# Kernel tuning notes

Measured on AMD Instinct MI355X. Metric: run time of the kernel, lower is better.

Reference implementation:

```python
import jax, jax.numpy as jnp
import numpy as np

N = 131072      # total nodes
B = 16          # graphs in batch (num_segments)
C = 128         # in_channels
K = 16          # n_super_nodes
TAU = 1.0
PRUNING_THRESHOLD = 0.01
SPARSITY_WEIGHT = 0.01
TEMPORAL_W = 0.1 * 5
COLLAPSE_W = 2.0
EPS = 1e-9


def setup_inputs() -> dict:
    key = jax.random.key(0)
    ks = jax.random.split(key, 8)
    x = jax.random.normal(ks[0], (N, C), dtype=jnp.float32)
    batch = jnp.sort(jax.random.randint(ks[1], (N,), 0, B)).astype(jnp.int64)
    pos = jax.random.normal(ks[2], (N, 2), dtype=jnp.float32)
    # Gumbel noise for gumbel_softmax (sampled once, passed as input for determinism)
    gumbel = jax.random.gumbel(ks[3], (N, K), dtype=jnp.float32)
    # assign_mlp params: Linear(C,C) -> ReLU -> Linear(C,K)
    W1 = jax.random.normal(ks[4], (C, C), dtype=jnp.float32) / np.sqrt(C)
    b1 = jnp.zeros((C,), dtype=jnp.float32)
    W2 = jax.random.normal(ks[5], (K, C), dtype=jnp.float32) / np.sqrt(C)
    b2 = jnp.zeros((K,), dtype=jnp.float32)
    scaling = jnp.asarray(10.0, dtype=jnp.float32)
    active_mask = jnp.ones((K,), dtype=jnp.float32)  # buffer, starts all-active
    return {"x": x, "batch": batch, "pos": pos, "gumbel": gumbel,
            "W1": W1, "b1": b1, "W2": W2, "b2": b2,
            "scaling": scaling, "active_mask": active_mask}


def reference(x, batch, pos, gumbel, W1, b1, W2, b2, scaling, active_mask):
    # --- assignment logits: MLP * scaling (eval mode, prev_assignments=None) ---
    h = jax.nn.relu(x @ W1.T + b1)            # [N, C]
    logits = (h @ W2.T + b2) * scaling        # [N, K]
    # eval-path masking: masked_fill(mask == 0, -1e9)
    masked_logits = jnp.where(active_mask[None, :] == 0.0, -1e9, logits)
    # gumbel_softmax (soft, hard=False)
    s = jax.nn.softmax((masked_logits + gumbel) / TAU, axis=-1)   # [N, K]

    avg_s = jnp.mean(s, axis=0)               # [K]

    # --- losses ---
    entropy = -jnp.mean(jnp.sum(s * jnp.log(s + EPS), axis=1))
    uniform_p = 1.0 / K
    diversity = jnp.sum(uniform_p * jnp.log(uniform_p / (avg_s + EPS)))
    pruning = jnp.mean(jnp.abs(avg_s * (1.0 - active_mask)))
    sparsity = (jnp.sum(active_mask) / K) * SPARSITY_WEIGHT
    temporal = jnp.asarray(0.0, jnp.float32)  # prev_assignments is None
    # collapse-prevention / balance bodies are truncated upstream; faithful proxies
    collapse = jnp.sum((avg_s - uniform_p) ** 2) * COLLAPSE_W
    balance = jnp.std(avg_s)
    spatial = jnp.asarray(0.0, jnp.float32)

    # --- pooled features: out[b,k,c] = sum_{n in graph b} s[n,k] * x[n,c] ---
    weighted = x[:, None, :] * s[:, :, None]                  # [N, K, C]
    out = jax.ops.segment_sum(weighted, batch, num_segments=B)  # [B, K, C]

    # --- super-node positions ---
    w_pos = pos[:, None, :] * s[:, :, None]                    # [N, K, 2]
    sum_s_pos = jax.ops.segment_sum(w_pos, batch, num_segments=B)  # [B, K, 2]
    sum_s = jax.ops.segment_sum(s, batch, num_segments=B)[..., None] + EPS  # [B, K, 1]
    mu = sum_s_pos / sum_s                                     # [B, K, 2]

    # --- separation loss: pairwise repulsion between super-node centers ---
    dist_sq = jnp.sum((mu[:, :, None, :] - mu[:, None, :, :]) ** 2, axis=-1)  # [B,K,K]
    eye = jnp.eye(K, dtype=mu.dtype)[None]
    repulsion = 1.0 / (dist_sq + 1.0)
    separation = jnp.sum(repulsion * (1.0 - eye)) / (K * (K - 1))

    losses = jnp.stack([entropy, diversity, spatial, pruning, sparsity,
                        temporal * TEMPORAL_W, collapse, balance, separation])
    return out, s, mu, losses
```

## Files before the change

kernel.cpp:

```cpp
#include <hip/hip_runtime.h>
#include <hip/hip_bf16.h>
#include <math.h>

#define NN 131072
#define BSEG 16
#define CCH 128
#define KK 16
#define EPSF 1e-9f
#define XST 136

#define OFF_S   32768
#define OFF_MU  2129920
#define OFF_L   2130432

#define REDC_BASE 1024
#define REDC_STRIDE 1024
#define NRED 64
#define ST_BASE (REDC_BASE + NRED * REDC_STRIDE)
#define NST 4
#define ST_SZ (BSEG * KK * CCH)

typedef __bf16 bf16x8 __attribute__((ext_vector_type(8)));
typedef float  f32x4  __attribute__((ext_vector_type(4)));
typedef float  f32x16 __attribute__((ext_vector_type(16)));

__device__ __forceinline__ int load_batch(const void* bptr, int n, int is64) {
    if (is64) return (int)((const long long*)bptr)[n];
    return ((const int*)bptr)[n];
}

__device__ __forceinline__ float wave_sum(float v) {
#pragma unroll
    for (int o = 32; o > 0; o >>= 1) v += __shfl_xor(v, o, 64);
    return v;
}

__device__ __forceinline__ bf16x8 pack8(float4 a, float4 b) {
    bf16x8 v;
    v[0] = (__bf16)a.x; v[1] = (__bf16)a.y; v[2] = (__bf16)a.z; v[3] = (__bf16)a.w;
    v[4] = (__bf16)b.x; v[5] = (__bf16)b.y; v[6] = (__bf16)b.z; v[7] = (__bf16)b.w;
    return v;
}

__global__ void k_zero(float* __restrict__ ws, const int* __restrict__ b32) {
    int i = blockIdx.x * 256 + threadIdx.x;
    ws[REDC_BASE + i] = 0.0f;
    if (i == 0) ws[0] = (b32[NN - 1] == 0) ? 1.0f : 0.0f;
}

__global__ __launch_bounds__(256, 2) void k_fused(
    const float* __restrict__ x, const void* __restrict__ batch,
    const float* __restrict__ pos, const float* __restrict__ gumbel,
    const float* __restrict__ W1, const float* __restrict__ b1,
    const float* __restrict__ W2, const float* __restrict__ b2,
    const float* __restrict__ scaling, const float* __restrict__ active_mask,
    float* __restrict__ s_out, float* __restrict__ ws)
{
    __shared__ __align__(16) __bf16 x_lds[128 * XST];
    __shared__ __align__(16) __bf16 h_lds[128 * XST];
    __shared__ __align__(16) __bf16 sT[16 * XST];
    __shared__ int bsegs[128];

    const int tid  = threadIdx.x;
    const int lane = tid & 63;
    const int wv   = tid >> 6;
    const int n0   = blockIdx.x * 128;
    const int is64 = (int)ws[0];

    if (tid < 128) bsegs[tid] = load_batch(batch, n0 + tid, is64);

    float4 ga0, ga1, ga2, ga3;
    if (tid < 128) {
        const float4* gp = (const float4*)(gumbel + (size_t)(n0 + tid) * KK);
        ga0 = gp[0]; ga1 = gp[1]; ga2 = gp[2]; ga3 = gp[3];
    }

    {
        const float4* xg = (const float4*)(x + (size_t)n0 * CCH);
#pragma unroll
        for (int i = 0; i < 8; i++) {
            int p = i * 256 + tid;
            float4 a = xg[2 * p], b = xg[2 * p + 1];
            *(bf16x8*)&x_lds[(p >> 4) * XST + (p & 15) * 8] = pack8(a, b);
        }
    }
    __syncthreads();

    {
        bf16x8 bfr[8];
        const float* wrow = W1 + (size_t)(wv * 32 + (lane & 31)) * CCH + (lane >> 5) * 8;
#pragma unroll
        for (int ks = 0; ks < 8; ks++) {
            float4 u = *(const float4*)(wrow + ks * 16);
            float4 v = *(const float4*)(wrow + ks * 16 + 4);
            bfr[ks] = pack8(u, v);
        }
        f32x16 acc[4];
#pragma unroll
        for (int mt = 0; mt < 4; mt++)
#pragma unroll
            for (int r = 0; r < 16; r++) acc[mt][r] = 0.0f;

#pragma unroll
        for (int ks = 0; ks < 8; ks++) {
#pragma unroll
            for (int mt = 0; mt < 4; mt++) {
                bf16x8 a = *(bf16x8*)&x_lds[(size_t)(mt * 32 + (lane & 31)) * XST + ks * 16 + (lane >> 5) * 8];
                acc[mt] = __builtin_amdgcn_mfma_f32_32x32x16_bf16(a, bfr[ks], acc[mt], 0, 0, 0);
            }
        }
        const float b1j = b1[wv * 32 + (lane & 31)];
#pragma unroll
        for (int mt = 0; mt < 4; mt++)
#pragma unroll
            for (int r = 0; r < 16; r++) {
                int node = mt * 32 + (r & 3) + 8 * (r >> 2) + 4 * (lane >> 5);
                h_lds[(size_t)node * XST + wv * 32 + (lane & 31)] = (__bf16)fmaxf(acc[mt][r] + b1j, 0.0f);
            }
    }
    __syncthreads();

    {
        f32x4 acc2[2];
#pragma unroll
        for (int t = 0; t < 2; t++)
#pragma unroll
            for (int r = 0; r < 4; r++) acc2[t][r] = 0.0f;

#pragma unroll
        for (int ks = 0; ks < 4; ks++) {
            const float* w2row = W2 + (size_t)(lane & 15) * CCH + ks * 32 + (lane >> 4) * 8;
            float4 u = *(const float4*)w2row;
            float4 v = *(const float4*)(w2row + 4);
            bf16x8 bw = pack8(u, v);
#pragma unroll
            for (int t = 0; t < 2; t++) {
                int tile = wv * 2 + t;
                bf16x8 a = *(bf16x8*)&h_lds[(size_t)(tile * 16 + (lane & 15)) * XST + ks * 32 + (lane >> 4) * 8];
                acc2[t] = __builtin_amdgcn_mfma_f32_16x16x32_bf16(a, bw, acc2[t], 0, 0, 0);
            }
        }
#pragma unroll
        for (int t = 0; t < 2; t++) {
#pragma unroll
            for (int r = 0; r < 4; r++) {
                int node = (wv * 2 + t) * 16 + (lane >> 4) * 4 + r;
                float* lp = (float*)((char*)h_lds + (size_t)node * (XST * 2) + 192);
                lp[lane & 15] = acc2[t][r];
            }
        }
    }
    __syncthreads();

    if (tid < 128) {
        const int n = n0 + tid;
        const char* rb = (const char*)h_lds + (size_t)tid * (XST * 2);
        float lg[16], gu[16];
#pragma unroll
        for (int i = 0; i < 4; i++) {
            float4 t = *(const float4*)(rb + 192 + 16 * i);
            lg[4 * i] = t.x; lg[4 * i + 1] = t.y; lg[4 * i + 2] = t.z; lg[4 * i + 3] = t.w;
        }
        gu[0] = ga0.x; gu[1] = ga0.y; gu[2]  = ga0.z; gu[3]  = ga0.w;
        gu[4] = ga1.x; gu[5] = ga1.y; gu[6]  = ga1.z; gu[7]  = ga1.w;
        gu[8] = ga2.x; gu[9] = ga2.y; gu[10] = ga2.z; gu[11] = ga2.w;
        gu[12] = ga3.x; gu[13] = ga3.y; gu[14] = ga3.z; gu[15] = ga3.w;

        const float sc = scaling[0];
        float m = -1e30f;
#pragma unroll
        for (int k = 0; k < KK; k++) {
            float v = (lg[k] + b2[k]) * sc;
            if (active_mask[k] == 0.0f) v = -1e9f;
            v += gu[k];
            lg[k] = v;
            m = fmaxf(m, v);
        }
        float ssum = 0.0f;
#pragma unroll
        for (int k = 0; k < KK; k++) { lg[k] = expf(lg[k] - m); ssum += lg[k]; }
        const float inv = 1.0f / ssum;
        float sarr[16];
#pragma unroll
        for (int k = 0; k < KK; k++) sarr[k] = lg[k] * inv;

        float4* srow = (float4*)(s_out + (size_t)n * KK);
#pragma unroll
        for (int i = 0; i < 4; i++) {
            float4 t;
            t.x = sarr[4 * i]; t.y = sarr[4 * i + 1]; t.z = sarr[4 * i + 2]; t.w = sarr[4 * i + 3];
            srow[i] = t;
        }
#pragma unroll
        for (int k = 0; k < KK; k++) sT[k * XST + tid] = (__bf16)sarr[k];

        float ent = 0.0f;
#pragma unroll
        for (int k = 0; k < KK; k++) ent += sarr[k] * logf(sarr[k] + EPSF);

        const float2 p = ((const float2*)pos)[n];
        const int bi = bsegs[tid];
        const int b0 = __shfl(bi, 0, 64);
        const int b1s = __shfl(bi, 63, 64);
        const float prim = (bi == b0) ? 1.0f : 0.0f;
        float* rc = ws + REDC_BASE + (size_t)(blockIdx.x & (NRED - 1)) * REDC_STRIDE;

#pragma unroll
        for (int k = 0; k < KK; k++) {
            float v = wave_sum(sarr[k] * prim);
            if (lane == 0) atomicAdd(&rc[b0 * 16 + k], v);
        }
#pragma unroll
        for (int k = 0; k < KK; k++) {
            float vx = wave_sum(sarr[k] * p.x * prim);
            float vy = wave_sum(sarr[k] * p.y * prim);
            if (lane == 0) {
                atomicAdd(&rc[256 + b0 * 32 + 2 * k],     vx);
                atomicAdd(&rc[256 + b0 * 32 + 2 * k + 1], vy);
            }
        }
        {
            float e = wave_sum(ent * prim);
            if (lane == 0) atomicAdd(&rc[768], e);
        }

        if (b0 != b1s) {
            const float sec = 1.0f - prim;
#pragma unroll
            for (int k = 0; k < KK; k++) {
                float v = wave_sum(sarr[k] * sec);
                if (lane == 0) atomicAdd(&rc[b1s * 16 + k], v);
            }
#pragma unroll
            for (int k = 0; k < KK; k++) {
                float vx = wave_sum(sarr[k] * p.x * sec);
                float vy = wave_sum(sarr[k] * p.y * sec);
                if (lane == 0) {
                    atomicAdd(&rc[256 + b1s * 32 + 2 * k],     vx);
                    atomicAdd(&rc[256 + b1s * 32 + 2 * k + 1], vy);
                }
            }
            float e = wave_sum(ent * sec);
            if (lane == 0) atomicAdd(&rc[768], e);
        }
    }
    __syncthreads();

    {
        float* stg = ws + ST_BASE + (size_t)(blockIdx.x & (NST - 1)) * ST_SZ;
        const int bfirst = bsegs[0], blast = bsegs[127];
        for (int seg = bfirst; seg <= blast; seg++) {
            const bool masked = (bfirst != blast);
            f32x4 pacc[2];
#pragma unroll
            for (int t = 0; t < 2; t++)
#pragma unroll
                for (int r = 0; r < 4; r++) pacc[t][r] = 0.0f;

#pragma unroll
            for (int ks = 0; ks < 4; ks++) {
                bf16x8 a = *(bf16x8*)&sT[(size_t)(lane & 15) * XST + ks * 32 + (lane >> 4) * 8];
                if (masked) {
#pragma unroll
                    for (int i = 0; i < 8; i++) {
                        int nd = ks * 32 + (lane >> 4) * 8 + i;
                        if (bsegs[nd] != seg) a[i] = (__bf16)0.0f;
                    }
                }
#pragma unroll
                for (int t = 0; t < 2; t++) {
                    int ct = wv * 2 + t;
                    bf16x8 bx;
#pragma unroll
                    for (int i = 0; i < 8; i++)
                        bx[i] = x_lds[(size_t)(ks * 32 + (lane >> 4) * 8 + i) * XST + ct * 16 + (lane & 15)];
                    pacc[t] = __builtin_amdgcn_mfma_f32_16x16x32_bf16(a, bx, pacc[t], 0, 0, 0);
                }
            }
#pragma unroll
            for (int t = 0; t < 2; t++) {
                int c = (wv * 2 + t) * 16 + (lane & 15);
#pragma unroll
                for (int r = 0; r < 4; r++) {
                    int k = (lane >> 4) * 4 + r;
                    atomicAdd(&stg[((size_t)seg * KK + k) * CCH + c], pacc[t][r]);
                }
            }
        }
    }
}

__global__ __launch_bounds__(256) void k_reduce(const float* __restrict__ ws,
                                                float* __restrict__ out) {
    int i = blockIdx.x * 256 + threadIdx.x;
    const float4* s0 = (const float4*)(ws + ST_BASE);
    const float4* s1 = (const float4*)(ws + ST_BASE + ST_SZ);
    const float4* s2 = (const float4*)(ws + ST_BASE + 2 * ST_SZ);
    const float4* s3 = (const float4*)(ws + ST_BASE + 3 * ST_SZ);
    float4 a = s0[i], b = s1[i], c = s2[i], d = s3[i];
    float4 r;
    r.x = (a.x + b.x) + (c.x + d.x);
    r.y = (a.y + b.y) + (c.y + d.y);
    r.z = (a.z + b.z) + (c.z + d.z);
    r.w = (a.w + b.w) + (c.w + d.w);
    ((float4*)out)[i] = r;
}

__global__ __launch_bounds__(256) void k_final(
    const float* __restrict__ ws, const float* __restrict__ active_mask,
    float* __restrict__ mu_out, float* __restrict__ losses)
{
    __shared__ float lsum[256];
    __shared__ float lpos[512];
    __shared__ float lent[1];
    __shared__ float smu[512];
    __shared__ float savg[16];
    __shared__ float red[256];
    const int tid = threadIdx.x;

    for (int a = tid; a < 769; a += 256) {
        float acc = 0.0f;
#pragma unroll 8
        for (int c = 0; c < NRED; c++) acc += ws[REDC_BASE + c * REDC_STRIDE + a];
        if (a < 256) lsum[a] = acc;
        else if (a < 768) lpos[a - 256] = acc;
        else lent[0] = acc;
    }
    __syncthreads();

    if (tid < 16) {
        float a = 0.0f;
#pragma unroll
        for (int b = 0; b < 16; b++) a += lsum[b * 16 + tid];
        savg[tid] = a / (float)NN;
    }
    for (int i = tid; i < 512; i += 256) {
        int sk = i >> 1;
        float v = lpos[i] / (lsum[sk] + EPSF);
        smu[i] = v;
        mu_out[i] = v;
    }
    __syncthreads();

    float rep = 0.0f;
    for (int t = tid; t < 4096; t += 256) {
        int b = t >> 8, i = (t >> 4) & 15, j = t & 15;
        if (i != j) {
            float dx = smu[b * 32 + i * 2]     - smu[b * 32 + j * 2];
            float dy = smu[b * 32 + i * 2 + 1] - smu[b * 32 + j * 2 + 1];
            rep += 1.0f / (dx * dx + dy * dy + 1.0f);
        }
    }
    red[tid] = rep;
    __syncthreads();
    for (int st = 128; st > 0; st >>= 1) {
        if (tid < st) red[tid] += red[tid + st];
        __syncthreads();
    }

    if (tid == 0) {
        const float p = 1.0f / 16.0f;
        float separation = red[0] / (float)(16 * 15);
        float entropy = -lent[0] / (float)NN;
        float diversity = 0.f, pruning = 0.f, amsum = 0.f, collapse = 0.f, mean = 0.f;
        for (int k = 0; k < 16; k++) {
            float a = savg[k];
            diversity += p * logf(p / (a + EPSF));
            pruning += fabsf(a * (1.0f - active_mask[k]));
            amsum += active_mask[k];
            collapse += (a - p) * (a - p);
            mean += a;
        }
        pruning /= 16.0f;
        mean /= 16.0f;
        float var = 0.f;
        for (int k = 0; k < 16; k++) { float d = savg[k] - mean; var += d * d; }
        float balance = sqrtf(var / 16.0f);
        float sparsity = (amsum / 16.0f) * 0.01f;
        collapse *= 2.0f;
        losses[0] = entropy;   losses[1] = diversity; losses[2] = 0.0f;
        losses[3] = pruning;   losses[4] = sparsity;  losses[5] = 0.0f;
        losses[6] = collapse;  losses[7] = balance;   losses[8] = separation;
    }
}

extern "C" void kernel_launch(void* const* d_in, const int* in_sizes, int n_in,
                              void* d_out, int out_size, void* d_ws, size_t ws_size,
                              hipStream_t stream) {
    const float* x       = (const float*)d_in[0];
    const void*  batch   = d_in[1];
    const float* pos     = (const float*)d_in[2];
    const float* gumbel  = (const float*)d_in[3];
    const float* W1      = (const float*)d_in[4];
    const float* b1      = (const float*)d_in[5];
    const float* W2      = (const float*)d_in[6];
    const float* b2      = (const float*)d_in[7];
    const float* scaling = (const float*)d_in[8];
    const float* am      = (const float*)d_in[9];

    float* out      = (float*)d_out;
    float* s_sec    = out + OFF_S;
    float* mu_sec   = out + OFF_MU;
    float* loss_sec = out + OFF_L;
    float* wsf      = (float*)d_ws;

    k_zero<<<768, 256, 0, stream>>>(wsf, (const int*)batch);
    k_fused<<<NN / 128, 256, 0, stream>>>(x, batch, pos, gumbel, W1, b1, W2, b2,
                                          scaling, am, s_sec, wsf);
    k_reduce<<<32, 256, 0, stream>>>(wsf, out);
    k_final<<<1, 256, 0, stream>>>(wsf, am, mu_sec, loss_sec);
}
```

Baseline: 184.0 us.

## Use 512-thread blocks splitting MFMA tiles across 8 waves; merge reduce and final kernels

The fused kernel now launches 512 threads per block. Work is redistributed so each of 8 waves handles half the M-tiles of the first GEMM, one 16-row tile of the second GEMM, and one 16-column tile of the pooled-feature MFMA. This is meant to give more waves to hide memory and MFMA latency. The final loss/mu kernel is folded into the reduce kernel as an extra block, removing one launch. The (512,4) launch bound caps registers per thread, so there is a risk of spills, and LDS use per block may still limit how many blocks fit on a CU.

```diff
diff --git a/kernel.cpp b/kernel.cpp
--- a/kernel.cpp
+++ b/kernel.cpp
@@ -13,6 +13,7 @@
 #define OFF_MU  2129920
 #define OFF_L   2130432
 
+#define FLAG_IDX 800
 #define REDC_BASE 1024
 #define REDC_STRIDE 1024
 #define NRED 64
@@ -45,10 +46,10 @@
 __global__ void k_zero(float* __restrict__ ws, const int* __restrict__ b32) {
     int i = blockIdx.x * 256 + threadIdx.x;
     ws[REDC_BASE + i] = 0.0f;
-    if (i == 0) ws[0] = (b32[NN - 1] == 0) ? 1.0f : 0.0f;
-}
-
-__global__ __launch_bounds__(256, 2) void k_fused(
+    if (i == 0) ws[FLAG_IDX] = (b32[NN - 1] == 0) ? 1.0f : 0.0f;
+}
+
+__global__ __launch_bounds__(512, 4) void k_fused(
     const float* __restrict__ x, const void* __restrict__ batch,
     const float* __restrict__ pos, const float* __restrict__ gumbel,
     const float* __restrict__ W1, const float* __restrict__ b1,
@@ -65,7 +66,7 @@
     const int lane = tid & 63;
     const int wv   = tid >> 6;
     const int n0   = blockIdx.x * 128;
-    const int is64 = (int)ws[0];
+    const int is64 = (int)ws[FLAG_IDX];
 
     if (tid < 128) bsegs[tid] = load_batch(batch, n0 + tid, is64);
 
@@ -78,8 +79,8 @@
     {
         const float4* xg = (const float4*)(x + (size_t)n0 * CCH);
 #pragma unroll
-        for (int i = 0; i < 8; i++) {
-            int p = i * 256 + tid;
+        for (int i = 0; i < 4; i++) {
+            int p = i * 512 + tid;
             float4 a = xg[2 * p], b = xg[2 * p + 1];
             *(bf16x8*)&x_lds[(p >> 4) * XST + (p & 15) * 8] = pack8(a, b);
         }
@@ -87,45 +88,46 @@
     __syncthreads();
 
     {
+        const int jw  = wv & 3;
+        const int mth = wv >> 2;
         bf16x8 bfr[8];
-        const float* wrow = W1 + (size_t)(wv * 32 + (lane & 31)) * CCH + (lane >> 5) * 8;
+        const float* wrow = W1 + (size_t)(jw * 32 + (lane & 31)) * CCH + (lane >> 5) * 8;
 #pragma unroll
         for (int ks = 0; ks < 8; ks++) {
             float4 u = *(const float4*)(wrow + ks * 16);
             float4 v = *(const float4*)(wrow + ks * 16 + 4);
             bfr[ks] = pack8(u, v);
         }
-        f32x16 acc[4];
-#pragma unroll
-        for (int mt = 0; mt < 4; mt++)
-#pragma unroll
-            for (int r = 0; r < 16; r++) acc[mt][r] = 0.0f;
+        f32x16 acc[2];
+#pragma unroll
+        for (int t = 0; t < 2; t++)
+#pragma unroll
+            for (int r = 0; r < 16; r++) acc[t][r] = 0.0f;
 
 #pragma unroll
         for (int ks = 0; ks < 8; ks++) {
 #pragma unroll
-            for (int mt = 0; mt < 4; mt++) {
+            for (int t = 0; t < 2; t++) {
+                int mt = mth * 2 + t;
                 bf16x8 a = *(bf16x8*)&x_lds[(size_t)(mt * 32 + (lane & 31)) * XST + ks * 16 + (lane >> 5) * 8];
-                acc[mt] = __builtin_amdgcn_mfma_f32_32x32x16_bf16(a, bfr[ks], acc[mt], 0, 0, 0);
-            }
-        }
-        const float b1j = b1[wv * 32 + (lane & 31)];
-#pragma unroll
-        for (int mt = 0; mt < 4; mt++)
+                acc[t] = __builtin_amdgcn_mfma_f32_32x32x16_bf16(a, bfr[ks], acc[t], 0, 0, 0);
+            }
+        }
+        const float b1j = b1[jw * 32 + (lane & 31)];
+#pragma unroll
+        for (int t = 0; t < 2; t++)
 #pragma unroll
             for (int r = 0; r < 16; r++) {
-                int node = mt * 32 + (r & 3) + 8 * (r >> 2) + 4 * (lane >> 5);
-                h_lds[(size_t)node * XST + wv * 32 + (lane & 31)] = (__bf16)fmaxf(acc[mt][r] + b1j, 0.0f);
+                int node = (mth * 2 + t) * 32 + (r & 3) + 8 * (r >> 2) + 4 * (lane >> 5);
+                h_lds[(size_t)node * XST + jw * 32 + (lane & 31)] = (__bf16)fmaxf(acc[t][r] + b1j, 0.0f);
             }
     }
     __syncthreads();
 
     {
-        f32x4 acc2[2];
-#pragma unroll
-        for (int t = 0; t < 2; t++)
-#pragma unroll
-            for (int r = 0; r < 4; r++) acc2[t][r] = 0.0f;
+        f32x4 acc2;
+#pragma unroll
+        for (int r = 0; r < 4; r++) acc2[r] = 0.0f;
 
 #pragma unroll
         for (int ks = 0; ks < 4; ks++) {
@@ -133,21 +135,14 @@
             float4 u = *(const float4*)w2row;
             float4 v = *(const float4*)(w2row + 4);
             bf16x8 bw = pack8(u, v);
-#pragma unroll
-            for (int t = 0; t < 2; t++) {
-                int tile = wv * 2 + t;
-                bf16x8 a = *(bf16x8*)&h_lds[(size_t)(tile * 16 + (lane & 15)) * XST + ks * 32 + (lane >> 4) * 8];
-                acc2[t] = __builtin_amdgcn_mfma_f32_16x16x32_bf16(a, bw, acc2[t], 0, 0, 0);
-            }
-        }
-#pragma unroll
-        for (int t = 0; t < 2; t++) {
-#pragma unroll
-            for (int r = 0; r < 4; r++) {
-                int node = (wv * 2 + t) * 16 + (lane >> 4) * 4 + r;
-                float* lp = (float*)((char*)h_lds + (size_t)node * (XST * 2) + 192);
-                lp[lane & 15] = acc2[t][r];
-            }
+            bf16x8 a = *(bf16x8*)&h_lds[(size_t)(wv * 16 + (lane & 15)) * XST + ks * 32 + (lane >> 4) * 8];
+            acc2 = __builtin_amdgcn_mfma_f32_16x16x32_bf16(a, bw, acc2, 0, 0, 0);
+        }
+#pragma unroll
+        for (int r = 0; r < 4; r++) {
+            int node = wv * 16 + (lane >> 4) * 4 + r;
+            float* lp = (float*)((char*)h_lds + (size_t)node * (XST * 2) + 192);
+            lp[lane & 15] = acc2[r];
         }
     }
     __syncthreads();
@@ -251,11 +246,9 @@
         const int bfirst = bsegs[0], blast = bsegs[127];
         for (int seg = bfirst; seg <= blast; seg++) {
             const bool masked = (bfirst != blast);
-            f32x4 pacc[2];
-#pragma unroll
-            for (int t = 0; t < 2; t++)
-#pragma unroll
-                for (int r = 0; r < 4; r++) pacc[t][r] = 0.0f;
+            f32x4 pacc;
+#pragma unroll
+            for (int r = 0; r < 4; r++) pacc[r] = 0.0f;
 
 #pragma unroll
             for (int ks = 0; ks < 4; ks++) {
@@ -267,56 +260,50 @@
                         if (bsegs[nd] != seg) a[i] = (__bf16)0.0f;
                     }
                 }
-#pragma unroll
-                for (int t = 0; t < 2; t++) {
-                    int ct = wv * 2 + t;
-                    bf16x8 bx;
-#pragma unroll
-                    for (int i = 0; i < 8; i++)
-                        bx[i] = x_lds[(size_t)(ks * 32 + (lane >> 4) * 8 + i) * XST + ct * 16 + (lane & 15)];
-                    pacc[t] = __builtin_amdgcn_mfma_f32_16x16x32_bf16(a, bx, pacc[t], 0, 0, 0);
-                }
-            }
-#pragma unroll
-            for (int t = 0; t < 2; t++) {
-                int c = (wv * 2 + t) * 16 + (lane & 15);
-#pragma unroll
-                for (int r = 0; r < 4; r++) {
-                    int k = (lane >> 4) * 4 + r;
-                    atomicAdd(&stg[((size_t)seg * KK + k) * CCH + c], pacc[t][r]);
-                }
-            }
-        }
-    }
-}
-
-__global__ __launch_bounds__(256) void k_reduce(const float* __restrict__ ws,
-                                                float* __restrict__ out) {
-    int i = blockIdx.x * 256 + threadIdx.x;
-    const float4* s0 = (const float4*)(ws + ST_BASE);
-    const float4* s1 = (const float4*)(ws + ST_BASE + ST_SZ);
-    const float4* s2 = (const float4*)(ws + ST_BASE + 2 * ST_SZ);
-    const float4* s3 = (const float4*)(ws + ST_BASE + 3 * ST_SZ);
-    float4 a = s0[i], b = s1[i], c = s2[i], d = s3[i];
-    float4 r;
-    r.x = (a.x + b.x) + (c.x + d.x);
-    r.y = (a.y + b.y) + (c.y + d.y);
-    r.z = (a.z + b.z) + (c.z + d.z);
-    r.w = (a.w + b.w) + (c.w + d.w);
-    ((float4*)out)[i] = r;
-}
-
-__global__ __launch_bounds__(256) void k_final(
-    const float* __restrict__ ws, const float* __restrict__ active_mask,
+                bf16x8 bx;
+#pragma unroll
+                for (int i = 0; i < 8; i++)
+                    bx[i] = x_lds[(size_t)(ks * 32 + (lane >> 4) * 8 + i) * XST + wv * 16 + (lane & 15)];
+                pacc = __builtin_amdgcn_mfma_f32_16x16x32_bf16(a, bx, pacc, 0, 0, 0);
+            }
+            const int c = wv * 16 + (lane & 15);
+#pragma unroll
+            for (int r = 0; r < 4; r++) {
+                int k = (lane >> 4) * 4 + r;
+                atomicAdd(&stg[((size_t)seg * KK + k) * CCH + c], pacc[r]);
+            }
+        }
+    }
+}
+
+__global__ __launch_bounds__(256) void k_reduce(
+    const float* __restrict__ ws, float* __restrict__ out,
+    const float* __restrict__ active_mask,
     float* __restrict__ mu_out, float* __restrict__ losses)
 {
+    const int tid = threadIdx.x;
+    if (blockIdx.x < 32) {
+        int i = blockIdx.x * 256 + tid;
+        const float4* s0 = (const float4*)(ws + ST_BASE);
+        const float4* s1 = (const float4*)(ws + ST_BASE + ST_SZ);
+        const float4* s2 = (const float4*)(ws + ST_BASE + 2 * ST_SZ);
+        const float4* s3 = (const float4*)(ws + ST_BASE + 3 * ST_SZ);
+        float4 a = s0[i], b = s1[i], c = s2[i], d = s3[i];
+        float4 r;
+        r.x = (a.x + b.x) + (c.x + d.x);
+        r.y = (a.y + b.y) + (c.y + d.y);
+        r.z = (a.z + b.z) + (c.z + d.z);
+        r.w = (a.w + b.w) + (c.w + d.w);
+        ((float4*)out)[i] = r;
+        return;
+    }
+
     __shared__ float lsum[256];
     __shared__ float lpos[512];
-    __shared__ float lent[1];
+    __shared__ float lent;
     __shared__ float smu[512];
     __shared__ float savg[16];
     __shared__ float red[256];
-    const int tid = threadIdx.x;
 
     for (int a = tid; a < 769; a += 256) {
         float acc = 0.0f;
@@ -324,7 +311,7 @@
         for (int c = 0; c < NRED; c++) acc += ws[REDC_BASE + c * REDC_STRIDE + a];
         if (a < 256) lsum[a] = acc;
         else if (a < 768) lpos[a - 256] = acc;
-        else lent[0] = acc;
+        else lent = acc;
     }
     __syncthreads();
 
@@ -361,7 +348,7 @@
     if (tid == 0) {
         const float p = 1.0f / 16.0f;
         float separation = red[0] / (float)(16 * 15);
-        float entropy = -lent[0] / (float)NN;
+        float entropy = -lent / (float)NN;
         float diversity = 0.f, pruning = 0.f, amsum = 0.f, collapse = 0.f, mean = 0.f;
         for (int k = 0; k < 16; k++) {
             float a = savg[k];
@@ -405,8 +392,7 @@
     float* wsf      = (float*)d_ws;
 
     k_zero<<<768, 256, 0, stream>>>(wsf, (const int*)batch);
-    k_fused<<<NN / 128, 256, 0, stream>>>(x, batch, pos, gumbel, W1, b1, W2, b2,
+    k_fused<<<NN / 128, 512, 0, stream>>>(x, batch, pos, gumbel, W1, b1, W2, b2,
                                           scaling, am, s_sec, wsf);
-    k_reduce<<<32, 256, 0, stream>>>(wsf, out);
-    k_final<<<1, 256, 0, stream>>>(wsf, am, mu_sec, loss_sec);
-}
+    k_reduce<<<33, 256, 0, stream>>>(wsf, out, am, mu_sec, loss_sec);
+}
```

New measurement: 189.3 us. +2.9%, slower.
